# Kernel tuning notes

Hardware: AMD Instinct MI355X
Metric: run time of the kernel (lower is better)

The kernel has to match this reference:

```python
import jax, jax.numpy as jnp
import numpy as np

LAYERS = [2048, 2048, 2048, 512]
THRESHOLD = 1.0
TAU_MEM = 20.0
TAU_SYN = 5.0
DT = 1.0
BATCH = 32
T = 100


def setup_inputs() -> dict:
    key = jax.random.key(0)
    ks = jax.random.split(key, 2 + 2 * (len(LAYERS) - 1))
    inp = {
        "x": jax.random.uniform(ks[0], (BATCH, LAYERS[0]), dtype=jnp.float32),
        "noise": jax.random.uniform(ks[1], (T, BATCH, LAYERS[0]), dtype=jnp.float32),
        "time_steps": T,
    }
    # nn.Linear-style init: U(-1/sqrt(fan_in), 1/sqrt(fan_in))
    for i in range(len(LAYERS) - 1):
        fan_in, fan_out = LAYERS[i], LAYERS[i + 1]
        bound = 1.0 / np.sqrt(fan_in)
        inp[f"W{i}"] = jax.random.uniform(ks[2 + 2 * i], (fan_out, fan_in), minval=-bound, maxval=bound, dtype=jnp.float32)
        inp[f"b{i}"] = jax.random.uniform(ks[3 + 2 * i], (fan_out,), minval=-bound, maxval=bound, dtype=jnp.float32)
    return inp


def _lif_step(I, mem, syn):
    # dI_syn/dt = -I_syn/tau_syn + I ; dV/dt = -V/tau_mem + I_syn  (explicit Euler, dt=1)
    syn = syn + (-syn / TAU_SYN + I) * DT
    mem = mem + (-mem / TAU_MEM + syn) * DT
    spikes = (mem >= THRESHOLD).astype(mem.dtype)
    mem = mem * (1.0 - spikes)          # reset fired neurons
    mem = mem * (mem > 0).astype(mem.dtype)  # clamp negative potentials to 0
    return spikes, mem, syn


def reference(x, noise, W0, b0, W1, b1, W2, b2, time_steps):
    params = [(W0, b0), (W1, b1), (W2, b2)]
    batch = x.shape[0]
    dtype = x.dtype
    rate = jnp.clip(x, 0.0, 1.0)                       # [B, in]
    in_spikes = (noise < rate[None]).astype(dtype)     # [T, B, in] Poisson encoding

    mems = tuple(jnp.zeros((batch, W.shape[0]), dtype) for W, _ in params)
    syns = tuple(jnp.zeros((batch, W.shape[0]), dtype) for W, _ in params)

    def step(carry, sp_in):
        mems, syns = carry
        layer_in = sp_in
        new_mems, new_syns = [], []
        count = jnp.zeros((), dtype)
        for (W, b), m, s in zip(params, mems, syns):
            I = layer_in @ W.T + b
            spk, m, s = _lif_step(I, m, s)
            new_mems.append(m)
            new_syns.append(s)
            count = count + spk.sum()
            layer_in = spk
        return (tuple(new_mems), tuple(new_syns)), (layer_in, count)

    (_, _), (out_spikes, counts) = jax.lax.scan(step, (mems, syns), in_spikes)
    output = out_spikes.mean(axis=0)   # [B, out]: time-averaged output spike train
    total_spikes = counts.sum()
    return output, total_spikes
```

## Files before the change

kernel.cpp:

```cpp
#include <hip/hip_runtime.h>

#define T_STEPS 100
#define MTOT    3200
#define R0_OFF  0
#define R1_OFF  13107200
#define I_OFF   26214400

typedef _Float16 half8_t __attribute__((ext_vector_type(8)));
typedef _Float16 half4_t __attribute__((ext_vector_type(4)));
typedef float    f32x4   __attribute__((ext_vector_type(4)));

__device__ __forceinline__ void encode_body(
    int blk, const float* __restrict__ x, const float* __restrict__ noise,
    _Float16* __restrict__ spk0, float* __restrict__ out)
{
    if (blk == 0 && threadIdx.x == 0) out[16384] = 0.0f;
    const int tid = threadIdx.x;
    const int m0  = blk * 16;
    __shared__ half8_t lds[16 * 257];
    #pragma unroll
    for (int ml = 0; ml < 16; ++ml) {
        const int m = m0 + ml;
        const int t = m >> 5, b = m & 31;
        const float4 x1 = *(const float4*)(x + b * 2048 + tid * 8);
        const float4 x2 = *(const float4*)(x + b * 2048 + tid * 8 + 4);
        const float4 n1 = *(const float4*)(noise + (size_t)t * 65536 + b * 2048 + tid * 8);
        const float4 n2 = *(const float4*)(noise + (size_t)t * 65536 + b * 2048 + tid * 8 + 4);
        const float xr[8] = {x1.x,x1.y,x1.z,x1.w,x2.x,x2.y,x2.z,x2.w};
        const float nz[8] = {n1.x,n1.y,n1.z,n1.w,n2.x,n2.y,n2.z,n2.w};
        half8_t sp;
        #pragma unroll
        for (int j = 0; j < 8; ++j) {
            const float r = fminf(fmaxf(xr[j], 0.0f), 1.0f);
            sp[j] = (nz[j] < r) ? (_Float16)1.0f : (_Float16)0.0f;
        }
        lds[ml * 257 + tid] = sp;
    }
    __syncthreads();
    #pragma unroll
    for (int r = 0; r < 16; ++r) {
        const int ml  = tid & 15;
        const int oct = r * 16 + (tid >> 4);
        *(half8_t*)(spk0 + ((size_t)oct * MTOT + m0 + ml) * 8) = lds[ml * 257 + oct];
    }
}

__device__ __forceinline__ void convw_body(
    int blk, const float* __restrict__ W, _Float16* __restrict__ Wf)
{
    const int koct = threadIdx.x;
    #pragma unroll
    for (int r = 0; r < 8; ++r) {
        const int row = blk * 8 + r;
        const float* wp = W + (size_t)row * 2048 + koct * 8;
        const float4 f1 = *(const float4*)(wp);
        const float4 f2 = *(const float4*)(wp + 4);
        half8_t h = {(_Float16)f1.x,(_Float16)f1.y,(_Float16)f1.z,(_Float16)f1.w,
                     (_Float16)f2.x,(_Float16)f2.y,(_Float16)f2.z,(_Float16)f2.w};
        const size_t idx = (size_t)(row >> 4) * 32768
                         + ((size_t)((koct >> 2) * 64 + (koct & 3) * 16 + (row & 15))) * 8;
        *(half8_t*)(Wf + idx) = h;
    }
}

__device__ __forceinline__ void scan_body(
    int blk, const _Float16* __restrict__ I, const float* __restrict__ bias,
    _Float16* __restrict__ spk_out, float* __restrict__ out,
    const int nshift, const int is_last)
{
    const int gid = blk * 256 + threadIdx.x;
    const int N = 1 << nshift;
    const int n = gid & (N - 1);
    const int b = gid >> nshift;
    const float bi = bias[n];
    const size_t nbase = (size_t)(n >> 3) * (MTOT * 8) + (n & 7);
    float mem = 0.f, syn = 0.f, osum = 0.f, cnt = 0.f;
    #pragma unroll 4
    for (int t = 0; t < T_STEPS; ++t) {
        const int m = t * 32 + b;
        const float Iv = (float)I[nbase + (size_t)m * 8] + bi;
        syn = syn + (-syn / 5.0f + Iv);
        mem = mem + (-mem / 20.0f + syn);
        const float sv = (mem >= 1.0f) ? 1.0f : 0.0f;
        mem = (sv != 0.0f) ? 0.0f : mem;
        mem = (mem > 0.0f) ? mem : 0.0f;
        cnt += sv; osum += sv;
        if (!is_last) spk_out[nbase + (size_t)m * 8] = (_Float16)sv;
    }
    if (is_last) out[b * 512 + n] = osum * 0.01f;
    float c = cnt;
    #pragma unroll
    for (int s2 = 1; s2 < 64; s2 <<= 1) c += __shfl_xor(c, s2);
    if ((threadIdx.x & 63) == 0) atomicAdd(&out[16384], c);
}

__global__ __launch_bounds__(256, 2) void snn_enc_convw_kernel(
    const float* __restrict__ x, const float* __restrict__ noise,
    _Float16* __restrict__ spk0, float* __restrict__ out,
    const float* __restrict__ W, _Float16* __restrict__ Wf)
{
    if (blockIdx.x < 200) encode_body(blockIdx.x, x, noise, spk0, out);
    else                  convw_body(blockIdx.x - 200, W, Wf);
}

__global__ __launch_bounds__(256, 4) void snn_scan_convw_kernel(
    const _Float16* __restrict__ I, const float* __restrict__ bias,
    _Float16* __restrict__ spk_out, float* __restrict__ out,
    const int scan_blocks, const int nshift,
    const float* __restrict__ W, _Float16* __restrict__ Wf)
{
    if ((int)blockIdx.x < scan_blocks)
        scan_body(blockIdx.x, I, bias, spk_out, out, nshift, 0);
    else
        convw_body(blockIdx.x - scan_blocks, W, Wf);
}

__global__ __launch_bounds__(256, 4) void snn_scan_kernel(
    const _Float16* __restrict__ I, const float* __restrict__ bias,
    float* __restrict__ out, const int nshift)
{
    scan_body(blockIdx.x, I, bias, nullptr, out, nshift, 1);
}


__device__ __forceinline__ half8_t ldB(const _Float16* __restrict__ p, int kq) {
    return *(const half8_t*)(p + (size_t)kq * (MTOT * 8));
}

__device__ __forceinline__ void stage_q(
    const _Float16* __restrict__ Wf, _Float16* __restrict__ wlds,
    const int nbb, const int q, const int w, const int lane)
{
    #pragma unroll
    for (int r = 0; r < 8; ++r) {
        const int unit = r * 512 + w * 64 + lane;
        const int s = unit >> 10, off = unit & 1023;
        const _Float16* src = Wf + (size_t)(4 * nbb + s) * 32768
                            + (size_t)q * 8192 + (size_t)off * 8;
        _Float16* dst = wlds + (size_t)unit * 8;
        __builtin_amdgcn_global_load_lds(
            (const __attribute__((address_space(1))) void*)src,
            (__attribute__((address_space(3))) void*)dst, 16, 0, 0);
    }
}

template<bool HAS2>
__device__ __forceinline__ void kstep512(
    const _Float16* __restrict__ wlds, const _Float16* const (&bp)[2],
    half8_t (&bb)[2], f32x4 (&acc)[2][4],
    const int lane, const int quad, const int kb, const int j)
{
    half8_t a[4];
    #pragma unroll
    for (int s = 0; s < 4; ++s)
        a[s] = *(const half8_t*)(wlds + (size_t)s * 8192 + (size_t)(j * 64 + lane) * 8);
    #pragma unroll
    for (int s = 0; s < 4; ++s) {
        acc[0][s] = __builtin_amdgcn_mfma_f32_16x16x32_f16(a[s], bb[0], acc[0][s], 0, 0, 0);
        if (HAS2)
            acc[1][s] = __builtin_amdgcn_mfma_f32_16x16x32_f16(a[s], bb[1], acc[1][s], 0, 0, 0);
    }
    if (kb + 2 < 64) {
        const int kq = (kb + 2) * 4 + quad;
        bb[0] = ldB(bp[0], kq);
        if (HAS2) bb[1] = ldB(bp[1], kq);
    }
}

template<bool HAS2>
__device__ __forceinline__ void gemm64s_run(
    const _Float16* __restrict__ Wf, const _Float16* __restrict__ spk,
    _Float16* __restrict__ I, _Float16* __restrict__ wlds,
    const int (&mt)[2], const int nbb, const int row_base,
    const int w, const int lane, const int quad, const int mi)
{
    const _Float16* bp[2];
    bp[0] = spk + ((size_t)mt[0] * 16 + mi) * 8;
    bp[1] = spk + ((size_t)mt[1] * 16 + mi) * 8;

    half8_t bE[2], bO[2];
    bE[0] = ldB(bp[0], quad);
    bO[0] = ldB(bp[0], 4 + quad);
    if (HAS2) { bE[1] = ldB(bp[1], quad); bO[1] = ldB(bp[1], 4 + quad); }

    stage_q(Wf, wlds, nbb, 0, w, lane);
    __syncthreads();

    f32x4 acc[2][4];
    #pragma unroll
    for (int u = 0; u < 2; ++u) {
        #pragma unroll
        for (int s = 0; s < 4; ++s) acc[u][s] = (f32x4){0, 0, 0, 0};
    }

    #pragma unroll 1
    for (int q = 0; q < 4; ++q) {
        #pragma unroll
        for (int j = 0; j < 16; j += 2) {
            kstep512<HAS2>(wlds, bp, bE, acc, lane, quad, q * 16 + j,     j);
            kstep512<HAS2>(wlds, bp, bO, acc, lane, quad, q * 16 + j + 1, j + 1);
        }
        __syncthreads();
        if (q < 3) {
            stage_q(Wf, wlds, nbb, q + 1, w, lane);
            __syncthreads();
        }
    }

    #pragma unroll
    for (int s = 0; s < 4; ++s) {
        const int n0 = row_base + s * 16 + quad * 4;
        const size_t obase = (size_t)(n0 >> 3) * (MTOT * 8) + (n0 & 7);
        #pragma unroll
        for (int u = 0; u < 2; ++u) {
            if (u == 1 && !HAS2) continue;
            half4_t h;
            #pragma unroll
            for (int r = 0; r < 4; ++r) h[r] = (_Float16)acc[u][s][r];
            *(half4_t*)(I + obase + (size_t)(mt[u] * 16 + mi) * 8) = h;
        }
    }
}

__global__ __launch_bounds__(512, 4) void snn_gemm64s_kernel(
    const _Float16* __restrict__ Wf, const _Float16* __restrict__ spk,
    _Float16* __restrict__ I)
{
    const int tid  = threadIdx.x;
    const int lane = tid & 63;
    const int w    = tid >> 6;
    const int mi   = lane & 15;
    const int quad = lane >> 4;
    const int chunk = blockIdx.x & 7;
    const int msl   = (blockIdx.x >> 3) & 1;
    const int nbb   = blockIdx.x >> 4;
    const int row_base = nbb * 64;
    const int jbase  = msl ? 13 : 0;
    const int jcount = msl ? 12 : 13;
    const int rem    = jcount - 8;
    const bool has2  = (w < rem);
    const int jl_start = jbase + (has2 ? 2 * w : w + rem);

    int mt[2];
    #pragma unroll
    for (int u = 0; u < 2; ++u) {
        int jl = jl_start + u;
        if (jl >= jbase + jcount) jl = jbase + jcount - 1;
        mt[u] = chunk + 8 * jl;
    }

    __shared__ _Float16 wlds[32768];

    if (has2) gemm64s_run<true >(Wf, spk, I, wlds, mt, nbb, row_base, w, lane, quad, mi);
    else      gemm64s_run<false>(Wf, spk, I, wlds, mt, nbb, row_base, w, lane, quad, mi);
}

template<int NC, int TPW>
__global__ __launch_bounds__(1024, 4) void snn_gemm_kernel(
    const _Float16* __restrict__ Wf, const _Float16* __restrict__ spk,
    _Float16* __restrict__ I)
{
    const int tid  = threadIdx.x;
    const int lane = tid & 63;
    const int w    = tid >> 6;
    const int quad = lane >> 4, mi = lane & 15;
    const int chunk = blockIdx.x % NC;
    const int nbb   = blockIdx.x / NC;
    const int row_base = nbb * 32;
    const int jcount = (200 - chunk + NC - 1) / NC;

    __shared__ _Float16 wlds[32 * 2048];
    {
        const half8_t* __restrict__ src = (const half8_t*)(Wf + (size_t)nbb * 65536);
        half8_t* __restrict__ dst = (half8_t*)wlds;
        #pragma unroll
        for (int r = 0; r < 8; ++r) dst[tid + r * 1024] = src[tid + r * 1024];
    }
    __syncthreads();

    for (int jl0 = TPW * w; jl0 < jcount; jl0 += 16 * TPW) {
        int mt[TPW]; bool val[TPW];
        const _Float16* bp[TPW];
        #pragma unroll
        for (int u = 0; u < TPW; ++u) {
            const int jl = jl0 + u;
            val[u] = jl < jcount;
            mt[u]  = chunk + NC * (val[u] ? jl : jl0);
            bp[u]  = spk + ((size_t)mt[u] * 16 + mi) * 8;
        }
        f32x4 acc[TPW][2];
        #pragma unroll
        for (int u = 0; u < TPW; ++u) { acc[u][0] = (f32x4){0,0,0,0}; acc[u][1] = (f32x4){0,0,0,0}; }

        half8_t bc[TPW];
        const size_t k0 = (size_t)quad * (MTOT * 8);
        #pragma unroll
        for (int u = 0; u < TPW; ++u) bc[u] = *(const half8_t*)(bp[u] + k0);

        #pragma unroll 4
        for (int kb = 0; kb < 64; ++kb) {
            half8_t bn[TPW];
            if (kb < 63) {
                const size_t kn = (size_t)((kb + 1) * 4 + quad) * (MTOT * 8);
                #pragma unroll
                for (int u = 0; u < TPW; ++u) bn[u] = *(const half8_t*)(bp[u] + kn);
            }
            const half8_t a0 = *(const half8_t*)(wlds + ((size_t)(kb * 64 + lane)) * 8);
            const half8_t a1 = *(const half8_t*)(wlds + 32768 + ((size_t)(kb * 64 + lane)) * 8);
            #pragma unroll
            for (int u = 0; u < TPW; ++u) {
                acc[u][0] = __builtin_amdgcn_mfma_f32_16x16x32_f16(a0, bc[u], acc[u][0], 0, 0, 0);
                acc[u][1] = __builtin_amdgcn_mfma_f32_16x16x32_f16(a1, bc[u], acc[u][1], 0, 0, 0);
            }
            #pragma unroll
            for (int u = 0; u < TPW; ++u) bc[u] = bn[u];
        }
        #pragma unroll
        for (int s = 0; s < 2; ++s) {
            const int n0 = row_base + s * 16 + quad * 4;
            const size_t obase = (size_t)(n0 >> 3) * (MTOT * 8) + (n0 & 7);
            #pragma unroll
            for (int u = 0; u < TPW; ++u) {
                if (!val[u]) continue;
                half4_t h;
                #pragma unroll
                for (int r = 0; r < 4; ++r) h[r] = (_Float16)acc[u][s][r];
                *(half4_t*)(I + obase + (size_t)(mt[u] * 16 + mi) * 8) = h;
            }
        }
    }
}

extern "C" void kernel_launch(void* const* d_in, const int* in_sizes, int n_in,
                              void* d_out, int out_size, void* d_ws, size_t ws_size,
                              hipStream_t stream) {
    const float* x     = (const float*)d_in[0];
    const float* noise = (const float*)d_in[1];
    const float* W0 = (const float*)d_in[3];
    const float* b0 = (const float*)d_in[4];
    const float* W1 = (const float*)d_in[5];
    const float* b1 = (const float*)d_in[6];
    const float* W2 = (const float*)d_in[7];
    const float* b2 = (const float*)d_in[8];
    float* out = (float*)d_out;

    _Float16* R0 = (_Float16*)((char*)d_ws + R0_OFF);
    _Float16* R1 = (_Float16*)((char*)d_ws + R1_OFF);
    _Float16* Ib = (_Float16*)((char*)d_ws + I_OFF);

    snn_enc_convw_kernel<<<dim3(456), dim3(256), 0, stream>>>(x, noise, R0, out, W0, R1);
    snn_gemm64s_kernel<<<dim3(512), dim3(512), 0, stream>>>(R1, R0, Ib);
    snn_scan_convw_kernel<<<dim3(512), dim3(256), 0, stream>>>(Ib, b0, R1, out, 256, 11, W1, R0);
    snn_gemm64s_kernel<<<dim3(512), dim3(512), 0, stream>>>(R0, R1, Ib);
    snn_scan_convw_kernel<<<dim3(320), dim3(256), 0, stream>>>(Ib, b1, R0, out, 256, 11, W2, R1);
    snn_gemm_kernel<16, 1><<<dim3(256), dim3(1024), 0, stream>>>(R1, R0, Ib);
    snn_scan_kernel<<<dim3(64), dim3(256), 0, stream>>>(Ib, b2, out, 9);

    (void)in_sizes; (void)n_in; (void)out_size; (void)ws_size;
}
```

Measured before the change: 274.8 us.

## Reuse staged 64-row GEMM for last layer and remap scan thread indexing

Replaces the separate last-layer GEMM (32-row tiles, whole weight slice held in LDS, 1024 threads) with the templated 64-row staged GEMM, parameterised by chunk count, split into M halves with guarded stores for idle waves. It also remaps scan threads so consecutive lanes cover 8 neurons of an octet across batches, which makes I reads and spike writes contiguous in the interleaved layout. The last layer now uses 256 blocks of 512 threads with quarter-staged weights. Edge-case handling for uneven chunk counts adds clamping logic and a possibly redundant tail.

```diff
diff --git a/kernel.cpp b/kernel.cpp
--- a/kernel.cpp
+++ b/kernel.cpp
@@ -69,11 +69,12 @@
     const int nshift, const int is_last)
 {
     const int gid = blk * 256 + threadIdx.x;
-    const int N = 1 << nshift;
-    const int n = gid & (N - 1);
-    const int b = gid >> nshift;
+    const int j   = gid & 7;
+    const int b   = (gid >> 3) & 31;
+    const int oct = gid >> 8;
+    const int n   = oct * 8 + j;
     const float bi = bias[n];
-    const size_t nbase = (size_t)(n >> 3) * (MTOT * 8) + (n & 7);
+    const size_t nbase = (size_t)oct * (MTOT * 8) + j;
     float mem = 0.f, syn = 0.f, osum = 0.f, cnt = 0.f;
     #pragma unroll 4
     for (int t = 0; t < T_STEPS; ++t) {
@@ -92,6 +93,7 @@
     #pragma unroll
     for (int s2 = 1; s2 < 64; s2 <<= 1) c += __shfl_xor(c, s2);
     if ((threadIdx.x & 63) == 0) atomicAdd(&out[16384], c);
+    (void)nshift;
 }
 
 __global__ __launch_bounds__(256, 2) void snn_enc_convw_kernel(
@@ -172,7 +174,8 @@
     const _Float16* __restrict__ Wf, const _Float16* __restrict__ spk,
     _Float16* __restrict__ I, _Float16* __restrict__ wlds,
     const int (&mt)[2], const int nbb, const int row_base,
-    const int w, const int lane, const int quad, const int mi)
+    const int w, const int lane, const int quad, const int mi,
+    const bool st)
 {
     const _Float16* bp[2];
     bp[0] = spk + ((size_t)mt[0] * 16 + mi) * 8;
@@ -213,6 +216,7 @@
         const size_t obase = (size_t)(n0 >> 3) * (MTOT * 8) + (n0 & 7);
         #pragma unroll
         for (int u = 0; u < 2; ++u) {
+            if (u == 0 && !st) continue;
             if (u == 1 && !HAS2) continue;
             half4_t h;
             #pragma unroll
@@ -222,6 +226,7 @@
     }
 }
 
+template<int NCHUNK>
 __global__ __launch_bounds__(512, 4) void snn_gemm64s_kernel(
     const _Float16* __restrict__ Wf, const _Float16* __restrict__ spk,
     _Float16* __restrict__ I)
@@ -231,104 +236,35 @@
     const int w    = tid >> 6;
     const int mi   = lane & 15;
     const int quad = lane >> 4;
-    const int chunk = blockIdx.x & 7;
-    const int msl   = (blockIdx.x >> 3) & 1;
-    const int nbb   = blockIdx.x >> 4;
+    const int chunk = blockIdx.x % NCHUNK;
+    const int rest  = blockIdx.x / NCHUNK;
+    const int msl   = rest & 1;
+    const int nbb   = rest >> 1;
     const int row_base = nbb * 64;
-    const int jbase  = msl ? 13 : 0;
-    const int jcount = msl ? 12 : 13;
+    const int jt     = (200 - chunk + NCHUNK - 1) / NCHUNK;
+    const int jh     = (jt + 1) >> 1;
+    const int jbase  = msl ? jh : 0;
+    const int jcount = msl ? (jt - jh) : jh;
     const int rem    = jcount - 8;
     const bool has2  = (w < rem);
-    const int jl_start = jbase + (has2 ? 2 * w : w + rem);
+    const int r2     = rem > 0 ? rem : 0;
+    const bool st    = has2 || (w + r2) < jcount;
+    int jl_start = jbase + (has2 ? 2 * w : w + r2);
+    const int jmax = jbase + jcount - 1;
+    if (jl_start > jmax) jl_start = jmax;
 
     int mt[2];
     #pragma unroll
     for (int u = 0; u < 2; ++u) {
         int jl = jl_start + u;
-        if (jl >= jbase + jcount) jl = jbase + jcount - 1;
-        mt[u] = chunk + 8 * jl;
+        if (jl > jmax) jl = jmax;
+        mt[u] = chunk + NCHUNK * jl;
     }
 
     __shared__ _Float16 wlds[32768];
 
-    if (has2) gemm64s_run<true >(Wf, spk, I, wlds, mt, nbb, row_base, w, lane, quad, mi);
-    else      gemm64s_run<false>(Wf, spk, I, wlds, mt, nbb, row_base, w, lane, quad, mi);
-}
-
-template<int NC, int TPW>
-__global__ __launch_bounds__(1024, 4) void snn_gemm_kernel(
-    const _Float16* __restrict__ Wf, const _Float16* __restrict__ spk,
-    _Float16* __restrict__ I)
-{
-    const int tid  = threadIdx.x;
-    const int lane = tid & 63;
-    const int w    = tid >> 6;
-    const int quad = lane >> 4, mi = lane & 15;
-    const int chunk = blockIdx.x % NC;
-    const int nbb   = blockIdx.x / NC;
-    const int row_base = nbb * 32;
-    const int jcount = (200 - chunk + NC - 1) / NC;
-
-    __shared__ _Float16 wlds[32 * 2048];
-    {
-        const half8_t* __restrict__ src = (const half8_t*)(Wf + (size_t)nbb * 65536);
-        half8_t* __restrict__ dst = (half8_t*)wlds;
-        #pragma unroll
-        for (int r = 0; r < 8; ++r) dst[tid + r * 1024] = src[tid + r * 1024];
-    }
-    __syncthreads();
-
-    for (int jl0 = TPW * w; jl0 < jcount; jl0 += 16 * TPW) {
-        int mt[TPW]; bool val[TPW];
-        const _Float16* bp[TPW];
-        #pragma unroll
-        for (int u = 0; u < TPW; ++u) {
-            const int jl = jl0 + u;
-            val[u] = jl < jcount;
-            mt[u]  = chunk + NC * (val[u] ? jl : jl0);
-            bp[u]  = spk + ((size_t)mt[u] * 16 + mi) * 8;
-        }
-        f32x4 acc[TPW][2];
-        #pragma unroll
-        for (int u = 0; u < TPW; ++u) { acc[u][0] = (f32x4){0,0,0,0}; acc[u][1] = (f32x4){0,0,0,0}; }
-
-        half8_t bc[TPW];
-        const size_t k0 = (size_t)quad * (MTOT * 8);
-        #pragma unroll
-        for (int u = 0; u < TPW; ++u) bc[u] = *(const half8_t*)(bp[u] + k0);
-
-        #pragma unroll 4
-        for (int kb = 0; kb < 64; ++kb) {
-            half8_t bn[TPW];
-            if (kb < 63) {
-                const size_t kn = (size_t)((kb + 1) * 4 + quad) * (MTOT * 8);
-                #pragma unroll
-                for (int u = 0; u < TPW; ++u) bn[u] = *(const half8_t*)(bp[u] + kn);
-            }
-            const half8_t a0 = *(const half8_t*)(wlds + ((size_t)(kb * 64 + lane)) * 8);
-            const half8_t a1 = *(const half8_t*)(wlds + 32768 + ((size_t)(kb * 64 + lane)) * 8);
-            #pragma unroll
-            for (int u = 0; u < TPW; ++u) {
-                acc[u][0] = __builtin_amdgcn_mfma_f32_16x16x32_f16(a0, bc[u], acc[u][0], 0, 0, 0);
-                acc[u][1] = __builtin_amdgcn_mfma_f32_16x16x32_f16(a1, bc[u], acc[u][1], 0, 0, 0);
-            }
-            #pragma unroll
-            for (int u = 0; u < TPW; ++u) bc[u] = bn[u];
-        }
-        #pragma unroll
-        for (int s = 0; s < 2; ++s) {
-            const int n0 = row_base + s * 16 + quad * 4;
-            const size_t obase = (size_t)(n0 >> 3) * (MTOT * 8) + (n0 & 7);
-            #pragma unroll
-            for (int u = 0; u < TPW; ++u) {
-                if (!val[u]) continue;
-                half4_t h;
-                #pragma unroll
-                for (int r = 0; r < 4; ++r) h[r] = (_Float16)acc[u][s][r];
-                *(half4_t*)(I + obase + (size_t)(mt[u] * 16 + mi) * 8) = h;
-            }
-        }
-    }
+    if (has2) gemm64s_run<true >(Wf, spk, I, wlds, mt, nbb, row_base, w, lane, quad, mi, true);
+    else      gemm64s_run<false>(Wf, spk, I, wlds, mt, nbb, row_base, w, lane, quad, mi, st);
 }
 
 extern "C" void kernel_launch(void* const* d_in, const int* in_sizes, int n_in,
@@ -349,11 +285,11 @@
     _Float16* Ib = (_Float16*)((char*)d_ws + I_OFF);
 
     snn_enc_convw_kernel<<<dim3(456), dim3(256), 0, stream>>>(x, noise, R0, out, W0, R1);
-    snn_gemm64s_kernel<<<dim3(512), dim3(512), 0, stream>>>(R1, R0, Ib);
+    snn_gemm64s_kernel<8><<<dim3(512), dim3(512), 0, stream>>>(R1, R0, Ib);
     snn_scan_convw_kernel<<<dim3(512), dim3(256), 0, stream>>>(Ib, b0, R1, out, 256, 11, W1, R0);
-    snn_gemm64s_kernel<<<dim3(512), dim3(512), 0, stream>>>(R0, R1, Ib);
+    snn_gemm64s_kernel<8><<<dim3(512), dim3(512), 0, stream>>>(R0, R1, Ib);
     snn_scan_convw_kernel<<<dim3(320), dim3(256), 0, stream>>>(Ib, b1, R0, out, 256, 11, W2, R1);
-    snn_gemm_kernel<16, 1><<<dim3(256), dim3(1024), 0, stream>>>(R1, R0, Ib);
+    snn_gemm64s_kernel<16><<<dim3(256), dim3(512), 0, stream>>>(R1, R0, Ib);
     snn_scan_kernel<<<dim3(64), dim3(256), 0, stream>>>(Ib, b2, out, 9);
 
     (void)in_sizes; (void)n_in; (void)out_size; (void)ws_size;
```

Measured after the change: 274.0 us. No clear change (-0.3%).
